# Performance work log

Hardware: AMD Instinct MI355X
Metric: run time of the kernel (lower is better)

## Reference

```python
import jax, jax.numpy as jnp
import numpy as np
from jax import lax

DIM = 512
HEADS = 8
HEAD_DIM = 64  # max(16, dim // num_heads)
INNER = HEADS * HEAD_DIM
REGION_SIZE = 32
EPEG_K = 5
SCALE = HEAD_DIM ** -0.5


def setup_inputs() -> dict:
    key = jax.random.key(0)
    ks = jax.random.split(key, 7)
    B, L = 1, 16384
    x = jax.random.normal(ks[0], (B, L, DIM), jnp.float32)
    qkv_w = jax.random.normal(ks[1], (3 * INNER, DIM), jnp.float32) * 0.02
    qkv_b = jax.random.normal(ks[2], (3 * INNER,), jnp.float32) * 0.02
    proj_w = jax.random.normal(ks[3], (DIM, INNER), jnp.float32) * 0.02
    proj_b = jax.random.normal(ks[4], (DIM,), jnp.float32) * 0.02
    epeg_w = jax.random.normal(ks[5], (HEADS, 1, EPEG_K, 1), jnp.float32) * 0.02
    epeg_b = jax.random.normal(ks[6], (HEADS,), jnp.float32) * 0.02
    return {"x": x, "qkv_w": qkv_w, "qkv_b": qkv_b, "proj_w": proj_w,
            "proj_b": proj_b, "epeg_w": epeg_w, "epeg_b": epeg_b}


def _forward(x, qkv_w, qkv_b, proj_w, proj_b, epeg_w, epeg_b):
    B, L, C = x.shape
    # _grid_pad: fold tokens onto square grid, pad to multiple of region_size
    Hs = int(np.ceil(np.sqrt(L)))
    Hs += (-Hs) % REGION_SIZE
    Ws = Hs
    r = REGION_SIZE
    add_len = Hs * Ws - L
    if add_len > 0:
        x = jnp.pad(x, ((0, 0), (0, add_len), (0, 0)))
    # region_partition: [B,H,W,C] -> [B*nW, r*r, C]
    xg = x.reshape(B, Hs // r, r, Ws // r, r, C)
    xg = xg.transpose(0, 1, 3, 2, 4, 5).reshape(-1, r * r, C)
    N = r * r
    # InnerAttention
    qkv = (xg @ qkv_w.T + qkv_b).reshape(-1, N, 3, HEADS, HEAD_DIM)
    qkv = qkv.transpose(2, 0, 3, 1, 4)  # [3, Bw, h, N, d]
    q, k, v = qkv[0], qkv[1], qkv[2]
    attn = jnp.einsum('bhid,bhjd->bhij', q * SCALE, k)  # [Bw, h, N, N]
    # EPEG: depthwise (k,1) conv over the attention-logit map
    pad = EPEG_K // 2
    conv = lax.conv_general_dilated(
        attn, epeg_w, window_strides=(1, 1),
        padding=((pad, pad), (0, 0)),
        dimension_numbers=('NCHW', 'OIHW', 'NCHW'),
        feature_group_count=HEADS) + epeg_b.reshape(1, HEADS, 1, 1)
    attn = jax.nn.softmax(attn + conv, axis=-1)
    out = jnp.einsum('bhij,bhjd->bhid', attn, v)  # [Bw, h, N, d]
    out = out.transpose(0, 2, 1, 3).reshape(-1, N, INNER)
    out = out @ proj_w.T + proj_b
    # region_reverse: [B*nW, r, r, C] -> [B, H*W, C]
    out = out.reshape(B, Hs // r, Ws // r, r, r, C)
    out = out.transpose(0, 1, 3, 2, 4, 5).reshape(B, Hs * Ws, C)
    if add_len > 0:
        out = out[:, :L]
    return out


def reference(x, qkv_w, qkv_b, proj_w, proj_b, epeg_w, epeg_b):
    return _forward(x, qkv_w, qkv_b, proj_w, proj_b, epeg_w, epeg_b)
```

## Files before the change

### kernel.cpp

```cpp
#include <hip/hip_runtime.h>


using bf16x8 = __attribute__((ext_vector_type(8))) short;
using f32x4  = __attribute__((ext_vector_type(4))) float;

__device__ __forceinline__ unsigned short f2bf(float f) {
    unsigned u = __float_as_uint(f);
    u += 0x7fff + ((u >> 16) & 1);
    return (unsigned short)(u >> 16);
}
__device__ __forceinline__ float bf2f(unsigned short s) {
    return __uint_as_float(((unsigned)s) << 16);
}
__device__ __forceinline__ unsigned cvtpk(float lo, float hi) {
    unsigned r;
    asm("v_cvt_pk_bf16_f32 %0, %1, %2" : "=v"(r) : "v"(lo), "v"(hi));
    return r;
}
__device__ __forceinline__ float fexp2(float x) {
    return __builtin_amdgcn_exp2f(x);
}
__device__ __forceinline__ void gload16(const void* g, void* l) {
    __builtin_amdgcn_global_load_lds(
        (const __attribute__((address_space(1))) void*)g,
        (__attribute__((address_space(3))) void*)l, 16, 0, 0);
}
__device__ __forceinline__ int l_from_rn(int region, int n) {
    int gi = region >> 2, gj = region & 3;
    int a = n >> 5, b = n & 31;
    return ((gi * 32 + a) << 7) + (gj << 5) + b;
}

__global__ __launch_bounds__(256) void cast_all_kernel(
    const float* __restrict__ x, const float* __restrict__ qkv_w,
    const float* __restrict__ proj_w, unsigned short* __restrict__ xb,
    unsigned short* __restrict__ wqkv, unsigned short* __restrict__ wproj)
{
    const int bid = blockIdx.x;
    const int tid = threadIdx.x;
    const float* src;
    unsigned short* dst;
    if (bid < 4096) {
        int t = bid * 4 + (tid >> 6);
        int c8 = tid & 63;
        int l = l_from_rn(t >> 10, t & 1023);
        src = x + (size_t)l * 512 + c8 * 8;
        dst = xb + (size_t)t * 512 + c8 * 8;
    } else if (bid < 4480) {
        size_t g = (size_t)(bid - 4096) * 256 + tid;
        src = qkv_w + g * 8;
        dst = wqkv + g * 8;
    } else {
        size_t g = (size_t)(bid - 4480) * 256 + tid;
        src = proj_w + g * 8;
        dst = wproj + g * 8;
    }
    float4 a = *(const float4*)src;
    float4 b = *(const float4*)(src + 4);
    bf16x8 o;
    o[0] = (short)f2bf(a.x); o[1] = (short)f2bf(a.y);
    o[2] = (short)f2bf(a.z); o[3] = (short)f2bf(a.w);
    o[4] = (short)f2bf(b.x); o[5] = (short)f2bf(b.y);
    o[6] = (short)f2bf(b.z); o[7] = (short)f2bf(b.w);
    *(bf16x8*)dst = o;
}

__global__ __launch_bounds__(256) void qkv_kernel(
    const unsigned short* __restrict__ xb, const unsigned short* __restrict__ wb,
    const float* __restrict__ bias, unsigned short* __restrict__ qo,
    unsigned short* __restrict__ ko, unsigned short* __restrict__ vto)
{
    __shared__ __align__(16) unsigned short As[128 * 64];
    __shared__ __align__(16) unsigned short Bs[128 * 64];
    const int c0t = blockIdx.x * 128;
    const int t0 = blockIdx.y * 128;
    const int tid = threadIdx.x;
    const int lane = tid & 63, w = tid >> 6;
    const int arow = lane & 15, kgrp = lane >> 4;
    const int wr = w >> 1, wc = w & 1;
    const int s = c0t >> 9;

    f32x4 acc[4][4];
    #pragma unroll
    for (int m = 0; m < 4; ++m)
        #pragma unroll
        for (int n = 0; n < 4; ++n) {
            f32x4 z = {0.f, 0.f, 0.f, 0.f};
            acc[m][n] = z;
        }

    for (int k0 = 0; k0 < 512; k0 += 64) {
        __syncthreads();
        #pragma unroll
        for (int it = 0; it < 4; ++it) {
            int slot = it * 256 + tid;
            int row = slot >> 3, phys = slot & 7;
            int c8 = phys ^ (row & 7);
            gload16(xb + (size_t)(t0 + row) * 512 + k0 + c8 * 8,
                    &As[(it * 256 + (w << 6)) * 8]);
            gload16(wb + (size_t)(c0t + row) * 512 + k0 + c8 * 8,
                    &Bs[(it * 256 + (w << 6)) * 8]);
        }
        __syncthreads();

        bf16x8 af[4][2], bfr[4][2];
        #pragma unroll
        for (int m = 0; m < 4; ++m) {
            int r = wr * 64 + m * 16 + arow;
            af[m][0] = *(const bf16x8*)&As[r * 64 + ((kgrp ^ (r & 7)) * 8)];
            af[m][1] = *(const bf16x8*)&As[r * 64 + (((4 + kgrp) ^ (r & 7)) * 8)];
        }
        #pragma unroll
        for (int n = 0; n < 4; ++n) {
            int r = wc * 64 + n * 16 + arow;
            bfr[n][0] = *(const bf16x8*)&Bs[r * 64 + ((kgrp ^ (r & 7)) * 8)];
            bfr[n][1] = *(const bf16x8*)&Bs[r * 64 + (((4 + kgrp) ^ (r & 7)) * 8)];
        }
        if (s < 2) {
            #pragma unroll
            for (int m = 0; m < 4; ++m)
                #pragma unroll
                for (int n = 0; n < 4; ++n) {
                    acc[m][n] = __builtin_amdgcn_mfma_f32_16x16x32_bf16(
                        af[m][0], bfr[n][0], acc[m][n], 0, 0, 0);
                    acc[m][n] = __builtin_amdgcn_mfma_f32_16x16x32_bf16(
                        af[m][1], bfr[n][1], acc[m][n], 0, 0, 0);
                }
        } else {
            #pragma unroll
            for (int m = 0; m < 4; ++m)
                #pragma unroll
                for (int n = 0; n < 4; ++n) {
                    acc[m][n] = __builtin_amdgcn_mfma_f32_16x16x32_bf16(
                        bfr[n][0], af[m][0], acc[m][n], 0, 0, 0);
                    acc[m][n] = __builtin_amdgcn_mfma_f32_16x16x32_bf16(
                        bfr[n][1], af[m][1], acc[m][n], 0, 0, 0);
                }
        }
    }

    const int region = t0 >> 10;
    const float qs = (s == 0) ? 0.18033688f : 1.0f;
    if (s < 2) {
        unsigned short* dst = (s == 0) ? qo : ko;
        #pragma unroll
        for (int n = 0; n < 4; ++n) {
            int cg = c0t + wc * 64 + n * 16 + arow;
            float bi = bias[cg];
            int h = (cg >> 6) & 7, d = cg & 63;
            #pragma unroll
            for (int m = 0; m < 4; ++m) {
                int tb = t0 + wr * 64 + m * 16 + kgrp * 4;
                unsigned short* p =
                    dst + ((size_t)(region * 8 + h) * 1024 + (tb & 1023)) * 64 + d;
                #pragma unroll
                for (int i = 0; i < 4; ++i)
                    p[(size_t)i * 64] = f2bf((acc[m][n][i] + bi) * qs);
            }
        }
    } else {
        #pragma unroll
        for (int n = 0; n < 4; ++n) {
            int cg0 = c0t + wc * 64 + n * 16 + kgrp * 4;
            float4 b4 = *(const float4*)&bias[cg0];
            int h = (cg0 & 511) >> 6;
            int d0 = cg0 & 63;
            #pragma unroll
            for (int m = 0; m < 4; ++m) {
                int tb = t0 + wr * 64 + m * 16 + arow;
                unsigned short* base = vto + (size_t)(region * 8 + h) * 65536 +
                                       (size_t)d0 * 1024 + (tb & 1023);
                base[0]    = f2bf(acc[m][n][0] + b4.x);
                base[1024] = f2bf(acc[m][n][1] + b4.y);
                base[2048] = f2bf(acc[m][n][2] + b4.z);
                base[3072] = f2bf(acc[m][n][3] + b4.w);
            }
        }
    }
}

__global__ __launch_bounds__(512) void attn_kernel(
    const unsigned short* __restrict__ qg, const unsigned short* __restrict__ kg,
    const unsigned short* __restrict__ vtg, const float* __restrict__ epw,
    const float* __restrict__ epb, unsigned short* __restrict__ ao)
{
    const int bid = blockIdx.x;
    const int wid = (bid & 7) * 64 + (bid >> 3);
    const int rb = wid & 3;
    const int rh = wid >> 2;
    const int head = rh & 7, region = rh >> 3;
    const unsigned short* qb = qg + (size_t)rh * 65536;
    const unsigned short* kb = kg + (size_t)rh * 65536;
    const unsigned short* vb = vtg + (size_t)rh * 65536;
    const int i0 = rb * 256;
    const int tid = threadIdx.x;
    const int lane = tid & 63, w = tid >> 6;
    const int arow = lane & 15, kgrp = lane >> 4;

    __shared__ __align__(16) unsigned short Ks[2][4096];
    __shared__ __align__(16) unsigned short VTs[2][4096];
    __shared__ __align__(16) unsigned short Ps[256 * 64];
    __shared__ float row_l[256];

    const int x0 = (kgrp ^ (arow & 7)) * 8;
    const int x1 = ((4 + kgrp) ^ (arow & 7)) * 8;
    int poff[4];
    #pragma unroll
    for (int ct = 0; ct < 4; ++ct)
        poff[ct] = (((2 * ct + (kgrp >> 1)) ^ (arow & 7)) << 4) + ((kgrp & 1) << 3);
    const int pr0 = (kgrp ^ (arow & 7)) << 4;
    const int pr1 = ((4 + kgrp) ^ (arow & 7)) << 4;
    const int plrow0 = w * 32 + arow;

    float c_[5];
    #pragma unroll
    for (int t = 0; t < 5; ++t) c_[t] = epw[head * 5 + t];
    c_[2] += 1.0f;

    bf16x8 qtf[2][2];
    #pragma unroll
    for (int m = 0; m < 2; ++m) {
        int gr = i0 + w * 32 + m * 16 + arow;
        float av[8], bv[8];
        #pragma unroll
        for (int e = 0; e < 8; ++e) { av[e] = 0.f; bv[e] = 0.f; }
        #pragma unroll
        for (int t = 0; t < 5; ++t) {
            int r = gr + t - 2;
            if (r >= 0 && r < 1024) {
                const unsigned short* p = qb + (size_t)r * 64 + kgrp * 8;
                bf16x8 a = *(const bf16x8*)p;
                bf16x8 b = *(const bf16x8*)(p + 32);
                float ct = c_[t];
                #pragma unroll
                for (int e = 0; e < 8; ++e) {
                    av[e] += ct * bf2f((unsigned short)a[e]);
                    bv[e] += ct * bf2f((unsigned short)b[e]);
                }
            }
        }
        union { unsigned u[4]; bf16x8 v; } pa, pb;
        #pragma unroll
        for (int e2 = 0; e2 < 4; ++e2) {
            pa.u[e2] = cvtpk(av[e2 * 2], av[e2 * 2 + 1]);
            pb.u[e2] = cvtpk(bv[e2 * 2], bv[e2 * 2 + 1]);
        }
        qtf[m][0] = pa.v;
        qtf[m][1] = pb.v;
    }

    f32x4 oacc[2][4];
    #pragma unroll
    for (int m = 0; m < 2; ++m)
        #pragma unroll
        for (int dt = 0; dt < 4; ++dt) {
            f32x4 z = {0.f, 0.f, 0.f, 0.f};
            oacc[m][dt] = z;
        }
    float lp[2] = {0.f, 0.f};

    auto stage = [&](int jt, int buf) {
        const int j0 = jt * 64;
        int row = tid >> 3, phys = tid & 7, c8 = phys ^ (row & 7);
        gload16(kb + (size_t)(j0 + row) * 64 + c8 * 8, &Ks[buf][w * 512]);
        gload16(vb + (size_t)row * 1024 + j0 + c8 * 8, &VTs[buf][w * 512]);
    };

    stage(0, 0);

    for (int jt = 0; jt < 16; ++jt) {
        const int cur = jt & 1;
        __syncthreads();
        if (jt < 15) stage(jt + 1, cur ^ 1);

        const unsigned short* Kc = &Ks[cur][0];
        const unsigned short* Vc = &VTs[cur][0];

        bf16x8 vf[4][2];
        #pragma unroll
        for (int dt = 0; dt < 4; ++dt) {
            int drow = dt * 16 + arow;
            vf[dt][0] = *(const bf16x8*)&Vc[drow * 64 + x0];
            vf[dt][1] = *(const bf16x8*)&Vc[drow * 64 + x1];
        }

        uint2 pu[4][2];
        __builtin_amdgcn_s_setprio(1);
        #pragma unroll
        for (int ct = 0; ct < 4; ++ct) {
            int krow = ct * 16 + arow;
            bf16x8 kf0 = *(const bf16x8*)&Kc[krow * 64 + x0];
            bf16x8 kf1 = *(const bf16x8*)&Kc[krow * 64 + x1];
            #pragma unroll
            for (int m = 0; m < 2; ++m) {
                f32x4 sacc = {0.f, 0.f, 0.f, 0.f};
                sacc = __builtin_amdgcn_mfma_f32_16x16x32_bf16(kf0, qtf[m][0], sacc, 0, 0, 0);
                sacc = __builtin_amdgcn_mfma_f32_16x16x32_bf16(kf1, qtf[m][1], sacc, 0, 0, 0);
                float p0 = fexp2(sacc[0]), p1 = fexp2(sacc[1]);
                float p2 = fexp2(sacc[2]), p3 = fexp2(sacc[3]);
                lp[m] += (p0 + p1) + (p2 + p3);
                pu[ct][m].x = cvtpk(p0, p1);
                pu[ct][m].y = cvtpk(p2, p3);
            }
        }
        __builtin_amdgcn_s_setprio(0);

        #pragma unroll
        for (int ct = 0; ct < 4; ++ct)
            #pragma unroll
            for (int m = 0; m < 2; ++m)
                *(uint2*)((char*)Ps + (plrow0 + m * 16) * 128 + poff[ct]) = pu[ct][m];
        __builtin_amdgcn_sched_barrier(0);
        __builtin_amdgcn_s_setprio(1);
        #pragma unroll
        for (int m = 0; m < 2; ++m) {
            const char* prow = (const char*)Ps + (plrow0 + m * 16) * 128;
            bf16x8 pf0 = *(const bf16x8*)(prow + pr0);
            bf16x8 pf1 = *(const bf16x8*)(prow + pr1);
            #pragma unroll
            for (int dt = 0; dt < 4; ++dt) {
                oacc[m][dt] = __builtin_amdgcn_mfma_f32_16x16x32_bf16(
                    pf0, vf[dt][0], oacc[m][dt], 0, 0, 0);
                oacc[m][dt] = __builtin_amdgcn_mfma_f32_16x16x32_bf16(
                    pf1, vf[dt][1], oacc[m][dt], 0, 0, 0);
            }
        }
        __builtin_amdgcn_s_setprio(0);
    }

    #pragma unroll
    for (int m = 0; m < 2; ++m) {
        float s = lp[m];
        s += __shfl_xor(s, 16);
        s += __shfl_xor(s, 32);
        if (kgrp == 0) row_l[w * 32 + m * 16 + arow] = s;
    }
    __syncthreads();
    #pragma unroll
    for (int m = 0; m < 2; ++m) {
        float inv[4];
        #pragma unroll
        for (int i = 0; i < 4; ++i)
            inv[i] = 1.f / row_l[w * 32 + m * 16 + kgrp * 4 + i];
        #pragma unroll
        for (int dt = 0; dt < 4; ++dt) {
            #pragma unroll
            for (int i = 0; i < 4; ++i) {
                size_t t = (size_t)region * 1024 + i0 + w * 32 + m * 16 + kgrp * 4 + i;
                ao[t * 512 + head * 64 + dt * 16 + arow] = f2bf(oacc[m][dt][i] * inv[i]);
            }
        }
    }
}

__global__ __launch_bounds__(256) void proj_kernel(
    const unsigned short* __restrict__ ab, const unsigned short* __restrict__ wb,
    const float* __restrict__ bias, float* __restrict__ out)
{
    __shared__ __align__(16) unsigned short As[128 * 64];
    __shared__ __align__(16) unsigned short Bs[128 * 64];
    const int c0t = blockIdx.x * 128;
    const int t0 = blockIdx.y * 128;
    const int tid = threadIdx.x;
    const int lane = tid & 63, w = tid >> 6;
    const int arow = lane & 15, kgrp = lane >> 4;
    const int wr = w >> 1, wc = w & 1;

    f32x4 acc[4][4];
    #pragma unroll
    for (int m = 0; m < 4; ++m)
        #pragma unroll
        for (int n = 0; n < 4; ++n) {
            f32x4 z = {0.f, 0.f, 0.f, 0.f};
            acc[m][n] = z;
        }

    for (int k0 = 0; k0 < 512; k0 += 64) {
        __syncthreads();
        #pragma unroll
        for (int it = 0; it < 4; ++it) {
            int slot = it * 256 + tid;
            int row = slot >> 3, phys = slot & 7;
            int c8 = phys ^ (row & 7);
            gload16(ab + (size_t)(t0 + row) * 512 + k0 + c8 * 8,
                    &As[(it * 256 + (w << 6)) * 8]);
            gload16(wb + (size_t)(c0t + row) * 512 + k0 + c8 * 8,
                    &Bs[(it * 256 + (w << 6)) * 8]);
        }
        __syncthreads();

        bf16x8 af[4][2], bfr[4][2];
        #pragma unroll
        for (int m = 0; m < 4; ++m) {
            int r = wr * 64 + m * 16 + arow;
            af[m][0] = *(const bf16x8*)&As[r * 64 + ((kgrp ^ (r & 7)) * 8)];
            af[m][1] = *(const bf16x8*)&As[r * 64 + (((4 + kgrp) ^ (r & 7)) * 8)];
        }
        #pragma unroll
        for (int n = 0; n < 4; ++n) {
            int r = wc * 64 + n * 16 + arow;
            bfr[n][0] = *(const bf16x8*)&Bs[r * 64 + ((kgrp ^ (r & 7)) * 8)];
            bfr[n][1] = *(const bf16x8*)&Bs[r * 64 + (((4 + kgrp) ^ (r & 7)) * 8)];
        }
        #pragma unroll
        for (int m = 0; m < 4; ++m)
            #pragma unroll
            for (int n = 0; n < 4; ++n) {
                acc[m][n] = __builtin_amdgcn_mfma_f32_16x16x32_bf16(
                    af[m][0], bfr[n][0], acc[m][n], 0, 0, 0);
                acc[m][n] = __builtin_amdgcn_mfma_f32_16x16x32_bf16(
                    af[m][1], bfr[n][1], acc[m][n], 0, 0, 0);
            }
    }

    #pragma unroll
    for (int n = 0; n < 4; ++n) {
        int cg = c0t + wc * 64 + n * 16 + arow;
        float bi = bias[cg];
        #pragma unroll
        for (int m = 0; m < 4; ++m) {
            int tb = t0 + wr * 64 + m * 16 + kgrp * 4;
            int l0 = l_from_rn(tb >> 10, tb & 1023);
            float* p = out + (size_t)l0 * 512 + cg;
            #pragma unroll
            for (int i = 0; i < 4; ++i)
                p[(size_t)i * 512] = acc[m][n][i] + bi;
        }
    }
}

extern "C" void kernel_launch(void* const* d_in, const int* in_sizes, int n_in,
                              void* d_out, int out_size, void* d_ws, size_t ws_size,
                              hipStream_t stream) {
    const float* x      = (const float*)d_in[0];
    const float* qkv_w  = (const float*)d_in[1];
    const float* qkv_b  = (const float*)d_in[2];
    const float* proj_w = (const float*)d_in[3];
    const float* proj_b = (const float*)d_in[4];
    const float* epeg_w = (const float*)d_in[5];
    const float* epeg_b = (const float*)d_in[6];
    float* out = (float*)d_out;

    const size_t NTOK = (size_t)16384 * 512;
    unsigned short* xb    = (unsigned short*)d_ws;
    unsigned short* wqkv  = xb + NTOK;
    unsigned short* wproj = wqkv + (size_t)1536 * 512;
    unsigned short* qb    = wproj + (size_t)512 * 512;
    unsigned short* kb    = qb + NTOK;
    unsigned short* vtb   = kb + NTOK;
    unsigned short* ao    = vtb + NTOK;

    cast_all_kernel<<<4608, 256, 0, stream>>>(x, qkv_w, proj_w, xb, wqkv, wproj);
    {
        dim3 grid(12, 128);
        qkv_kernel<<<grid, 256, 0, stream>>>(xb, wqkv, qkv_b, qb, kb, vtb);
    }
    attn_kernel<<<512, 512, 0, stream>>>(qb, kb, vtb, epeg_w, epeg_b, ao);
    {
        dim3 grid(4, 128);
        proj_kernel<<<grid, 256, 0, stream>>>(ao, wproj, proj_b, out);
    }
}
```

Measured before the change: 128.3 us.

## Keep P in registers by computing transposed PV MFMA, drop LDS round-trip

The attention kernel no longer writes the exponentiated scores P to shared memory and reads them back. It swaps operand roles in the PV MFMA (V^T fragment as A, P register fragment as B), so the output accumulator is transposed. V fragments are now gathered with a matching permuted k-ordering from two 8-byte LDS loads. The epilogue then normalizes per row without a shared row_l buffer or barrier and stores packed 4-element bf16 vectors. This removes the LDS traffic and barrier for P and cuts shared memory per block, which may raise occupancy, at the cost of more, smaller LDS reads for V.

```diff
diff --git a/kernel.cpp b/kernel.cpp
--- a/kernel.cpp
+++ b/kernel.cpp
@@ -199,18 +199,9 @@
 
     __shared__ __align__(16) unsigned short Ks[2][4096];
     __shared__ __align__(16) unsigned short VTs[2][4096];
-    __shared__ __align__(16) unsigned short Ps[256 * 64];
-    __shared__ float row_l[256];
 
     const int x0 = (kgrp ^ (arow & 7)) * 8;
     const int x1 = ((4 + kgrp) ^ (arow & 7)) * 8;
-    int poff[4];
-    #pragma unroll
-    for (int ct = 0; ct < 4; ++ct)
-        poff[ct] = (((2 * ct + (kgrp >> 1)) ^ (arow & 7)) << 4) + ((kgrp & 1) << 3);
-    const int pr0 = (kgrp ^ (arow & 7)) << 4;
-    const int pr1 = ((4 + kgrp) ^ (arow & 7)) << 4;
-    const int plrow0 = w * 32 + arow;
 
     float c_[5];
     #pragma unroll
@@ -276,12 +267,19 @@
         const unsigned short* Kc = &Ks[cur][0];
         const unsigned short* Vc = &VTs[cur][0];
 
-        bf16x8 vf[4][2];
+        bf16x8 vfa[4][2];
         #pragma unroll
         for (int dt = 0; dt < 4; ++dt) {
-            int drow = dt * 16 + arow;
-            vf[dt][0] = *(const bf16x8*)&Vc[drow * 64 + x0];
-            vf[dt][1] = *(const bf16x8*)&Vc[drow * 64 + x1];
+            const char* vrow = (const char*)Vc + (dt * 16 + arow) * 128;
+            #pragma unroll
+            for (int cp = 0; cp < 2; ++cp) {
+                union { uint2 u2[2]; bf16x8 v; } a;
+                int s0 = (cp * 4 + (kgrp >> 1)) ^ (arow & 7);
+                int s1 = (cp * 4 + 2 + (kgrp >> 1)) ^ (arow & 7);
+                a.u2[0] = *(const uint2*)(vrow + (s0 << 4) + ((kgrp & 1) << 3));
+                a.u2[1] = *(const uint2*)(vrow + (s1 << 4) + ((kgrp & 1) << 3));
+                vfa[dt][cp] = a.v;
+            }
         }
 
         uint2 pu[4][2];
@@ -303,26 +301,17 @@
                 pu[ct][m].y = cvtpk(p2, p3);
             }
         }
-        __builtin_amdgcn_s_setprio(0);
-
-        #pragma unroll
-        for (int ct = 0; ct < 4; ++ct)
-            #pragma unroll
-            for (int m = 0; m < 2; ++m)
-                *(uint2*)((char*)Ps + (plrow0 + m * 16) * 128 + poff[ct]) = pu[ct][m];
-        __builtin_amdgcn_sched_barrier(0);
-        __builtin_amdgcn_s_setprio(1);
         #pragma unroll
         for (int m = 0; m < 2; ++m) {
-            const char* prow = (const char*)Ps + (plrow0 + m * 16) * 128;
-            bf16x8 pf0 = *(const bf16x8*)(prow + pr0);
-            bf16x8 pf1 = *(const bf16x8*)(prow + pr1);
-            #pragma unroll
-            for (int dt = 0; dt < 4; ++dt) {
-                oacc[m][dt] = __builtin_amdgcn_mfma_f32_16x16x32_bf16(
-                    pf0, vf[dt][0], oacc[m][dt], 0, 0, 0);
-                oacc[m][dt] = __builtin_amdgcn_mfma_f32_16x16x32_bf16(
-                    pf1, vf[dt][1], oacc[m][dt], 0, 0, 0);
+            #pragma unroll
+            for (int cp = 0; cp < 2; ++cp) {
+                union { uint2 u2[2]; bf16x8 v; } pb;
+                pb.u2[0] = pu[2 * cp][m];
+                pb.u2[1] = pu[2 * cp + 1][m];
+                #pragma unroll
+                for (int dt = 0; dt < 4; ++dt)
+                    oacc[m][dt] = __builtin_amdgcn_mfma_f32_16x16x32_bf16(
+                        vfa[dt][cp], pb.v, oacc[m][dt], 0, 0, 0);
             }
         }
         __builtin_amdgcn_s_setprio(0);
@@ -333,22 +322,15 @@
         float s = lp[m];
         s += __shfl_xor(s, 16);
         s += __shfl_xor(s, 32);
-        if (kgrp == 0) row_l[w * 32 + m * 16 + arow] = s;
-    }
-    __syncthreads();
-    #pragma unroll
-    for (int m = 0; m < 2; ++m) {
-        float inv[4];
-        #pragma unroll
-        for (int i = 0; i < 4; ++i)
-            inv[i] = 1.f / row_l[w * 32 + m * 16 + kgrp * 4 + i];
+        float inv = 1.f / s;
+        size_t t = (size_t)region * 1024 + i0 + w * 32 + m * 16 + arow;
+        unsigned short* base = ao + t * 512 + head * 64;
         #pragma unroll
         for (int dt = 0; dt < 4; ++dt) {
-            #pragma unroll
-            for (int i = 0; i < 4; ++i) {
-                size_t t = (size_t)region * 1024 + i0 + w * 32 + m * 16 + kgrp * 4 + i;
-                ao[t * 512 + head * 64 + dt * 16 + arow] = f2bf(oacc[m][dt][i] * inv[i]);
-            }
+            uint2 o;
+            o.x = cvtpk(oacc[m][dt][0] * inv, oacc[m][dt][1] * inv);
+            o.y = cvtpk(oacc[m][dt][2] * inv, oacc[m][dt][3] * inv);
+            *(uint2*)(base + dt * 16 + kgrp * 4) = o;
         }
     }
 }
```

Result: slower. 135.7 us (+5.7%).
